# Kernel tuning notes

Measured on AMD Instinct MI355X. Metric: run time of the kernel, lower is better.

Reference implementation:

```python
import jax, jax.numpy as jnp
import numpy as np

HIDDEN = 160
LAYERS = 32
CLASSES = 10
IN_DIM = 784


def setup_inputs() -> dict:
    key = jax.random.key(0)
    ks = jax.random.split(key, 6)
    B = 65536
    x = jax.random.normal(ks[0], (B, IN_DIM), dtype=jnp.float32)
    # embed: torch nn.Linear(IN_DIM, HIDDEN); store weight as [IN_DIM, HIDDEN] so y = x @ W + b
    embed_w = jax.random.normal(ks[1], (IN_DIM, HIDDEN), dtype=jnp.float32) / np.sqrt(IN_DIM)
    embed_b = jnp.zeros((HIDDEN,), dtype=jnp.float32)
    # 32 residual-layer weights, kaiming_normal (fan_in=HIDDEN, relu gain sqrt(2)) scaled by 0.1
    layer_w = jax.random.normal(ks[2], (LAYERS, HIDDEN, HIDDEN), dtype=jnp.float32) * (np.sqrt(2.0 / HIDDEN) * 0.1)
    head_w = jax.random.normal(ks[3], (HIDDEN, CLASSES), dtype=jnp.float32) / np.sqrt(HIDDEN)
    head_b = jnp.zeros((CLASSES,), dtype=jnp.float32)
    return {"x": x, "embed_w": embed_w, "embed_b": embed_b,
            "layer_w": layer_w, "head_w": head_w, "head_b": head_b}


def reference(x, embed_w, embed_b, layer_w, head_w, head_b):
    # x: [B, 784] (already flat)
    h = x @ embed_w + embed_b  # [B, H]

    def step(h, W):
        # y = relu(h @ W) + h
        return jax.nn.relu(h @ W) + h, None

    h, _ = jax.lax.scan(step, h, layer_w)  # scan over the 32 layer weights
    return h @ head_w + head_b  # [B, CLASSES]
```

## Files before the change

### kernel.cpp

```cpp
#include <hip/hip_runtime.h>
#include <cstdint>
#include <cstddef>


typedef __attribute__((ext_vector_type(8))) short bfrag8;
typedef __attribute__((ext_vector_type(16))) float f32x16;
typedef __attribute__((ext_vector_type(4))) uint32_t u32x4;

#define MFMA32(a, b, c) __builtin_amdgcn_mfma_f32_32x32x16_bf16((a), (b), (c), 0, 0, 0)

#define NFRAG_TOTAL 1855
#define HALF_BYTES  25600
#define HALF_ELEMS  12800

#define WAITVM(N) asm volatile("s_waitcnt vmcnt(" #N ")" ::: "memory")

static __device__ __forceinline__ uint16_t f2bf16u(float v) {
    uint32_t u = __builtin_bit_cast(uint32_t, v);
    uint32_t r = u + 0x7FFFu + ((u >> 16) & 1u);
    return (uint16_t)(r >> 16);
}
static __device__ __forceinline__ uint32_t pack2_bf16(float lo, float hi) {
    return (uint32_t)f2bf16u(lo) | ((uint32_t)f2bf16u(hi) << 16);
}
static __device__ __forceinline__ uint32_t cvtpk(float lo, float hi) {
    uint32_t r;
    asm("v_cvt_pk_bf16_f32 %0, %1, %2" : "=v"(r) : "v"(lo), "v"(hi));
    return r;
}
static __device__ __forceinline__ void gl_lds16(const void* g, void* l) {
    __builtin_amdgcn_global_load_lds(
        (const __attribute__((address_space(1))) uint32_t*)g,
        (__attribute__((address_space(3))) uint32_t*)l, 16, 0, 0);
}

__global__ __launch_bounds__(256) void resmlp_prep(
    const float* __restrict__ embed_w, const float* __restrict__ layer_w,
    const float* __restrict__ head_w, uint16_t* __restrict__ ws)
{
    const int fb = blockIdx.x * 4 + (threadIdx.x >> 6);
    if (fb >= NFRAG_TOTAL) return;
    const int l = threadIdx.x & 63;
    const int h = l >> 5, m32 = l & 31;
    float v[8];
    if (fb < 245) {
        const int kt = fb / 5, mt = fb % 5;
        const int m = mt * 32 + m32;
        const int kb = kt * 16 + h * 8;
#pragma unroll
        for (int j = 0; j < 8; ++j)
            v[j] = embed_w[(size_t)(kb + j) * 160 + m];
    } else if (fb < 1845) {
        const int t = fb - 245, L = t / 50, r = t % 50, kt = r / 5, mt = r % 5;
        const int m = mt * 32 + m32;
        const float* W = layer_w + (size_t)L * 25600;
        const int kb = 32 * (kt >> 1) + 16 * (kt & 1) + 4 * h;
#pragma unroll
        for (int j = 0; j < 8; ++j)
            v[j] = W[(size_t)(kb + (j & 3) + 8 * (j >> 2)) * 160 + m];
    } else {
        const int kt = fb - 1845;
        const int kb = 32 * (kt >> 1) + 16 * (kt & 1) + 4 * h;
#pragma unroll
        for (int j = 0; j < 8; ++j)
            v[j] = (m32 < 10) ? head_w[(kb + (j & 3) + 8 * (j >> 2)) * 10 + m32] : 0.f;
    }
    u32x4 wv;
    wv.x = pack2_bf16(v[0], v[1]);
    wv.y = pack2_bf16(v[2], v[3]);
    wv.z = pack2_bf16(v[4], v[5]);
    wv.w = pack2_bf16(v[6], v[7]);
    *(u32x4*)((char*)ws + (size_t)fb * 1024 + l * 16) = wv;
}

template<int NK>
static __device__ __forceinline__ void embed_loadx(const float* __restrict__ xb,
                                                   float4 (&xv)[10])
{
#pragma unroll
    for (int kt = 0; kt < NK; ++kt) {
        xv[2 * kt]     = *(const float4*)(xb + kt * 16);
        xv[2 * kt + 1] = *(const float4*)(xb + kt * 16 + 4);
    }
}

template<int NK>
static __device__ __forceinline__ void embed_mfma_h(
    const uint16_t* __restrict__ buf, const float4 (&xv)[10],
    f32x16 (&acc)[5], int lane8)
{
    __builtin_amdgcn_s_setprio(1);
#pragma unroll
    for (int kt = 0; kt < NK; ++kt) {
        const float4 v0 = xv[2 * kt], v1 = xv[2 * kt + 1];
        u32x4 bw;
        bw.x = cvtpk(v0.x, v0.y);
        bw.y = cvtpk(v0.z, v0.w);
        bw.z = cvtpk(v1.x, v1.y);
        bw.w = cvtpk(v1.z, v1.w);
        const bfrag8 b = __builtin_bit_cast(bfrag8, bw);
#pragma unroll
        for (int mt = 0; mt < 5; ++mt) {
            const bfrag8 a = *(const bfrag8*)(buf + (kt * 5 + mt) * 512 + lane8);
            acc[mt] = MFMA32(a, b, acc[mt]);
        }
    }
    __builtin_amdgcn_s_setprio(0);
}

template<int KT0, int NMT, bool ZC>
static __device__ __forceinline__ void layer_mfma_h(
    const uint16_t* __restrict__ buf, f32x16 (&acc)[5],
    const f32x16 (&resid)[5], int lane8)
{
    __builtin_amdgcn_s_setprio(1);
#pragma unroll
    for (int i = 0; i < 5; ++i) {
        const int kt = KT0 + i, ms = kt >> 1, rb = (kt & 1) * 8;
        u32x4 bw;
        bw.x = cvtpk(resid[ms][rb + 0], resid[ms][rb + 1]);
        bw.y = cvtpk(resid[ms][rb + 2], resid[ms][rb + 3]);
        bw.z = cvtpk(resid[ms][rb + 4], resid[ms][rb + 5]);
        bw.w = cvtpk(resid[ms][rb + 6], resid[ms][rb + 7]);
        const bfrag8 b = __builtin_bit_cast(bfrag8, bw);
#pragma unroll
        for (int mt = 0; mt < NMT; ++mt) {
            const bfrag8 a = *(const bfrag8*)(buf + (i * NMT + mt) * 512 + lane8);
            if (ZC && i == 0) {
                f32x16 z;
#pragma unroll
                for (int r = 0; r < 16; ++r) z[r] = 0.f;
                acc[mt] = MFMA32(a, b, z);
            } else {
                acc[mt] = MFMA32(a, b, acc[mt]);
            }
        }
    }
    __builtin_amdgcn_s_setprio(0);
}

__global__ __launch_bounds__(256, 2) void resmlp_main(
    const float* __restrict__ x,
    const float* __restrict__ embed_b,
    const float* __restrict__ head_b,
    const uint16_t* __restrict__ ws,
    float* __restrict__ out)
{
    extern __shared__ __align__(16) uint16_t lds[];
    const int tid  = threadIdx.x;
    const int wave = tid >> 6, lane = tid & 63;
    const int hi = lane >> 5;
    const int lane8 = lane * 8;
    const int batch = blockIdx.x * 128 + wave * 32 + (lane & 31);

    f32x16 acc[5], resid[5];
#pragma unroll
    for (int mt = 0; mt < 5; ++mt)
#pragma unroll
        for (int r = 0; r < 16; ++r) acc[mt][r] = 0.f;

    auto do_stage = [&](int u) {
        int S, C;
        if (u < 10)      { S = (u >> 1) * 50 + (u & 1) * 25; C = (u == 9) ? 20 : 25; }
        else if (u < 74) { S = 245 + (u - 10) * 25;          C = 25; }
        else             { S = 1845 + (u - 74) * 5;          C = 5; }
        const char* src = (const char*)ws + (size_t)S * 1024 + lane * 16;
        char* dst = (char*)lds + (u % 3) * HALF_BYTES + lane * 16;
        for (int i = wave; i < C; i += 4)
            gl_lds16(src + (size_t)i * 1024, dst + i * 1024);
    };

    do_stage(0);
    do_stage(1);

    const float* xrow = x + (size_t)batch * 784 + hi * 8;

    for (int c = 0; c < 5; ++c) {
        float4 xv[10];
        __builtin_amdgcn_s_barrier();
        embed_loadx<5>(xrow + c * 160, xv);
        do_stage(2 * c + 2);
        WAITVM(11);
        embed_mfma_h<5>(lds + ((2 * c) % 3) * HALF_ELEMS, xv, acc, lane8);
        __builtin_amdgcn_s_barrier();
        if (c < 4) embed_loadx<5>(xrow + c * 160 + 80, xv);
        else       embed_loadx<4>(xrow + c * 160 + 80, xv);
        do_stage(2 * c + 3);
        WAITVM(11);
        if (c < 4) embed_mfma_h<5>(lds + ((2 * c + 1) % 3) * HALF_ELEMS, xv, acc, lane8);
        else       embed_mfma_h<4>(lds + ((2 * c + 1) % 3) * HALF_ELEMS, xv, acc, lane8);
    }

    for (int L = 0; L < 31; ++L) {
        const int u = 10 + 2 * L;
        const int bA = u % 3, bB = (u + 1) % 3;
        __builtin_amdgcn_s_barrier();
        do_stage(u + 2);
        if (L == 0) {
#pragma unroll
            for (int mt = 0; mt < 5; ++mt)
#pragma unroll
                for (int q2 = 0; q2 < 4; ++q2) {
                    const float4 b4 = *(const float4*)(embed_b + mt * 32 + q2 * 8 + hi * 4);
                    resid[mt][q2 * 4 + 0] = acc[mt][q2 * 4 + 0] + b4.x;
                    resid[mt][q2 * 4 + 1] = acc[mt][q2 * 4 + 1] + b4.y;
                    resid[mt][q2 * 4 + 2] = acc[mt][q2 * 4 + 2] + b4.z;
                    resid[mt][q2 * 4 + 3] = acc[mt][q2 * 4 + 3] + b4.w;
                }
        } else {
#pragma unroll
            for (int mt = 0; mt < 5; ++mt)
#pragma unroll
                for (int r = 0; r < 16; ++r)
                    resid[mt][r] += fmaxf(acc[mt][r], 0.f);
        }
        WAITVM(12);
        layer_mfma_h<0, 5, true>(lds + bA * HALF_ELEMS, acc, resid, lane8);
        __builtin_amdgcn_s_barrier();
        do_stage(u + 3);
        WAITVM(12);
        layer_mfma_h<5, 5, false>(lds + bB * HALF_ELEMS, acc, resid, lane8);
    }

    {
        __builtin_amdgcn_s_barrier();
        do_stage(74);
#pragma unroll
        for (int mt = 0; mt < 5; ++mt)
#pragma unroll
            for (int r = 0; r < 16; ++r)
                resid[mt][r] += fmaxf(acc[mt][r], 0.f);
        WAITVM(7);
        layer_mfma_h<0, 5, true>(lds + 0 * HALF_ELEMS, acc, resid, lane8);
        __builtin_amdgcn_s_barrier();
        do_stage(75);
        WAITVM(2);
        layer_mfma_h<5, 5, false>(lds + 1 * HALF_ELEMS, acc, resid, lane8);
    }

    {
        __builtin_amdgcn_s_barrier();
#pragma unroll
        for (int mt = 0; mt < 5; ++mt)
#pragma unroll
            for (int r = 0; r < 16; ++r)
                resid[mt][r] += fmaxf(acc[mt][r], 0.f);
        WAITVM(1);
        layer_mfma_h<0, 1, true>(lds + 2 * HALF_ELEMS, acc, resid, lane8);
        __builtin_amdgcn_s_barrier();
        WAITVM(0);
        layer_mfma_h<5, 1, false>(lds + 0 * HALF_ELEMS, acc, resid, lane8);
    }

    float* op = out + (size_t)batch * 10;
    if (hi == 0) {
        op[0] = acc[0][0] + head_b[0];
        op[1] = acc[0][1] + head_b[1];
        op[2] = acc[0][2] + head_b[2];
        op[3] = acc[0][3] + head_b[3];
        op[8] = acc[0][4] + head_b[8];
        op[9] = acc[0][5] + head_b[9];
    } else {
        op[4] = acc[0][0] + head_b[4];
        op[5] = acc[0][1] + head_b[5];
        op[6] = acc[0][2] + head_b[6];
        op[7] = acc[0][3] + head_b[7];
    }
}

extern "C" void kernel_launch(void* const* d_in, const int* in_sizes, int n_in,
                              void* d_out, int out_size, void* d_ws, size_t ws_size,
                              hipStream_t stream) {
    (void)in_sizes; (void)n_in; (void)out_size; (void)ws_size;
    const float* x       = (const float*)d_in[0];
    const float* embed_w = (const float*)d_in[1];
    const float* embed_b = (const float*)d_in[2];
    const float* layer_w = (const float*)d_in[3];
    const float* head_w  = (const float*)d_in[4];
    const float* head_b  = (const float*)d_in[5];
    float* out = (float*)d_out;

    uint16_t* ws = (uint16_t*)d_ws;

    const int dynLds = 3 * HALF_BYTES;
    (void)hipFuncSetAttribute((const void*)resmlp_main,
                              hipFuncAttributeMaxDynamicSharedMemorySize, dynLds);

    resmlp_prep<<<(NFRAG_TOTAL + 3) / 4, 256, 0, stream>>>(embed_w, layer_w, head_w, ws);
    resmlp_main<<<512, 256, dynLds, stream>>>(x, embed_b, head_b, ws, out);
}
```

Before: 398.8 us.

## Process two 32-row batch tiles per wave to reuse weight fragments across MFMAs

Each wave now handles 64 batch rows as two 32-row sub-tiles, so every LDS weight fragment read feeds two MFMAs instead of one. The block covers 256 rows, the grid is halved to 256 blocks, and occupancy drops to one block per CU. The LDS ring grows from three to six slots so a whole layer is staged ahead with one barrier per layer instead of two. In exchange, accumulator and residual register use roughly doubles, and the lower occupancy and single-block-per-CU schedule may expose more latency. The s_setprio hints are also removed.

```diff
diff --git a/kernel.cpp b/kernel.cpp
--- a/kernel.cpp
+++ b/kernel.cpp
@@ -10,8 +10,8 @@
 #define MFMA32(a, b, c) __builtin_amdgcn_mfma_f32_32x32x16_bf16((a), (b), (c), 0, 0, 0)
 
 #define NFRAG_TOTAL 1855
-#define HALF_BYTES  25600
-#define HALF_ELEMS  12800
+#define SLOT_BYTES  25600
+#define SLOT_ELEMS  12800
 
 #define WAITVM(N) asm volatile("s_waitcnt vmcnt(" #N ")" ::: "memory")
 
@@ -73,73 +73,68 @@
     *(u32x4*)((char*)ws + (size_t)fb * 1024 + l * 16) = wv;
 }
 
-template<int NK>
-static __device__ __forceinline__ void embed_loadx(const float* __restrict__ xb,
-                                                   float4 (&xv)[10])
-{
-#pragma unroll
-    for (int kt = 0; kt < NK; ++kt) {
-        xv[2 * kt]     = *(const float4*)(xb + kt * 16);
-        xv[2 * kt + 1] = *(const float4*)(xb + kt * 16 + 4);
-    }
-}
-
-template<int NK>
-static __device__ __forceinline__ void embed_mfma_h(
-    const uint16_t* __restrict__ buf, const float4 (&xv)[10],
-    f32x16 (&acc)[5], int lane8)
-{
-    __builtin_amdgcn_s_setprio(1);
-#pragma unroll
-    for (int kt = 0; kt < NK; ++kt) {
-        const float4 v0 = xv[2 * kt], v1 = xv[2 * kt + 1];
-        u32x4 bw;
-        bw.x = cvtpk(v0.x, v0.y);
-        bw.y = cvtpk(v0.z, v0.w);
-        bw.z = cvtpk(v1.x, v1.y);
-        bw.w = cvtpk(v1.z, v1.w);
-        const bfrag8 b = __builtin_bit_cast(bfrag8, bw);
+template<int NKT>
+static __device__ __forceinline__ void embed_half(
+    const uint16_t* __restrict__ buf,
+    const float* __restrict__ xr0, const float* __restrict__ xr1,
+    int kb, f32x16 (&acc)[2][5], int lane8)
+{
+#pragma unroll
+    for (int kt = 0; kt < NKT; ++kt) {
+        const float4 a0 = *(const float4*)(xr0 + kb + kt * 16);
+        const float4 a1 = *(const float4*)(xr0 + kb + kt * 16 + 4);
+        const float4 c0 = *(const float4*)(xr1 + kb + kt * 16);
+        const float4 c1 = *(const float4*)(xr1 + kb + kt * 16 + 4);
+        u32x4 w0, w1;
+        w0.x = cvtpk(a0.x, a0.y); w0.y = cvtpk(a0.z, a0.w);
+        w0.z = cvtpk(a1.x, a1.y); w0.w = cvtpk(a1.z, a1.w);
+        w1.x = cvtpk(c0.x, c0.y); w1.y = cvtpk(c0.z, c0.w);
+        w1.z = cvtpk(c1.x, c1.y); w1.w = cvtpk(c1.z, c1.w);
+        const bfrag8 b0 = __builtin_bit_cast(bfrag8, w0);
+        const bfrag8 b1 = __builtin_bit_cast(bfrag8, w1);
 #pragma unroll
         for (int mt = 0; mt < 5; ++mt) {
             const bfrag8 a = *(const bfrag8*)(buf + (kt * 5 + mt) * 512 + lane8);
-            acc[mt] = MFMA32(a, b, acc[mt]);
-        }
-    }
-    __builtin_amdgcn_s_setprio(0);
-}
-
-template<int KT0, int NMT, bool ZC>
-static __device__ __forceinline__ void layer_mfma_h(
-    const uint16_t* __restrict__ buf, f32x16 (&acc)[5],
-    const f32x16 (&resid)[5], int lane8)
-{
-    __builtin_amdgcn_s_setprio(1);
+            acc[0][mt] = MFMA32(a, b0, acc[0][mt]);
+            acc[1][mt] = MFMA32(a, b1, acc[1][mt]);
+        }
+    }
+}
+
+template<int KTB, int NMT, bool ZC>
+static __device__ __forceinline__ void layer_half(
+    const uint16_t* __restrict__ buf, f32x16 (&acc)[2][5],
+    const f32x16 (&resid)[2][5], const f32x16& zf, int lane8)
+{
 #pragma unroll
     for (int i = 0; i < 5; ++i) {
-        const int kt = KT0 + i, ms = kt >> 1, rb = (kt & 1) * 8;
-        u32x4 bw;
-        bw.x = cvtpk(resid[ms][rb + 0], resid[ms][rb + 1]);
-        bw.y = cvtpk(resid[ms][rb + 2], resid[ms][rb + 3]);
-        bw.z = cvtpk(resid[ms][rb + 4], resid[ms][rb + 5]);
-        bw.w = cvtpk(resid[ms][rb + 6], resid[ms][rb + 7]);
-        const bfrag8 b = __builtin_bit_cast(bfrag8, bw);
+        const int kt = KTB + i, ms = kt >> 1, rb = (kt & 1) * 8;
+        u32x4 w0, w1;
+        w0.x = cvtpk(resid[0][ms][rb + 0], resid[0][ms][rb + 1]);
+        w0.y = cvtpk(resid[0][ms][rb + 2], resid[0][ms][rb + 3]);
+        w0.z = cvtpk(resid[0][ms][rb + 4], resid[0][ms][rb + 5]);
+        w0.w = cvtpk(resid[0][ms][rb + 6], resid[0][ms][rb + 7]);
+        w1.x = cvtpk(resid[1][ms][rb + 0], resid[1][ms][rb + 1]);
+        w1.y = cvtpk(resid[1][ms][rb + 2], resid[1][ms][rb + 3]);
+        w1.z = cvtpk(resid[1][ms][rb + 4], resid[1][ms][rb + 5]);
+        w1.w = cvtpk(resid[1][ms][rb + 6], resid[1][ms][rb + 7]);
+        const bfrag8 b0 = __builtin_bit_cast(bfrag8, w0);
+        const bfrag8 b1 = __builtin_bit_cast(bfrag8, w1);
 #pragma unroll
         for (int mt = 0; mt < NMT; ++mt) {
             const bfrag8 a = *(const bfrag8*)(buf + (i * NMT + mt) * 512 + lane8);
             if (ZC && i == 0) {
-                f32x16 z;
-#pragma unroll
-                for (int r = 0; r < 16; ++r) z[r] = 0.f;
-                acc[mt] = MFMA32(a, b, z);
+                acc[0][mt] = MFMA32(a, b0, zf);
+                acc[1][mt] = MFMA32(a, b1, zf);
             } else {
-                acc[mt] = MFMA32(a, b, acc[mt]);
+                acc[0][mt] = MFMA32(a, b0, acc[0][mt]);
+                acc[1][mt] = MFMA32(a, b1, acc[1][mt]);
             }
         }
     }
-    __builtin_amdgcn_s_setprio(0);
-}
-
-__global__ __launch_bounds__(256, 2) void resmlp_main(
+}
+
+__global__ __launch_bounds__(256, 1) void resmlp_main(
     const float* __restrict__ x,
     const float* __restrict__ embed_b,
     const float* __restrict__ head_b,
@@ -149,122 +144,122 @@
     extern __shared__ __align__(16) uint16_t lds[];
     const int tid  = threadIdx.x;
     const int wave = tid >> 6, lane = tid & 63;
-    const int hi = lane >> 5;
+    const int hi = lane >> 5, ln = lane & 31;
     const int lane8 = lane * 8;
-    const int batch = blockIdx.x * 128 + wave * 32 + (lane & 31);
-
-    f32x16 acc[5], resid[5];
-#pragma unroll
-    for (int mt = 0; mt < 5; ++mt)
-#pragma unroll
-        for (int r = 0; r < 16; ++r) acc[mt][r] = 0.f;
-
-    auto do_stage = [&](int u) {
+    const int batch0 = blockIdx.x * 256 + wave * 64;
+    const float* xr0 = x + (size_t)(batch0 + ln) * 784 + hi * 8;
+    const float* xr1 = xr0 + (size_t)32 * 784;
+
+    f32x16 acc[2][5], resid[2][5];
+#pragma unroll
+    for (int s = 0; s < 2; ++s)
+#pragma unroll
+        for (int mt = 0; mt < 5; ++mt)
+#pragma unroll
+            for (int r = 0; r < 16; ++r) acc[s][mt][r] = 0.f;
+    f32x16 zf;
+#pragma unroll
+    for (int r = 0; r < 16; ++r) zf[r] = 0.f;
+
+    auto do_stage = [&](int u, int slot) {
         int S, C;
         if (u < 10)      { S = (u >> 1) * 50 + (u & 1) * 25; C = (u == 9) ? 20 : 25; }
         else if (u < 74) { S = 245 + (u - 10) * 25;          C = 25; }
-        else             { S = 1845 + (u - 74) * 5;          C = 5; }
+        else             { S = 1845 + (u - 74) * 5;          C = 5;  }
         const char* src = (const char*)ws + (size_t)S * 1024 + lane * 16;
-        char* dst = (char*)lds + (u % 3) * HALF_BYTES + lane * 16;
+        char* dst = (char*)lds + (size_t)slot * SLOT_BYTES + lane * 16;
         for (int i = wave; i < C; i += 4)
             gl_lds16(src + (size_t)i * 1024, dst + i * 1024);
     };
 
-    do_stage(0);
-    do_stage(1);
-
-    const float* xrow = x + (size_t)batch * 784 + hi * 8;
-
-    for (int c = 0; c < 5; ++c) {
-        float4 xv[10];
+    do_stage(0, 0);
+    WAITVM(0);
+    __builtin_amdgcn_s_barrier();
+
+    for (int e = 0; e < 8; ++e) {
+        do_stage(e + 1, (e + 1) % 6);
+        embed_half<5>(lds + (e % 6) * SLOT_ELEMS, xr0, xr1, e * 80, acc, lane8);
+        WAITVM(0);
         __builtin_amdgcn_s_barrier();
-        embed_loadx<5>(xrow + c * 160, xv);
-        do_stage(2 * c + 2);
-        WAITVM(11);
-        embed_mfma_h<5>(lds + ((2 * c) % 3) * HALF_ELEMS, xv, acc, lane8);
+    }
+    do_stage(9, 3);
+    embed_half<5>(lds + 2 * SLOT_ELEMS, xr0, xr1, 640, acc, lane8);
+    do_stage(10, 4);
+    do_stage(11, 5);
+    WAITVM(12);
+    __builtin_amdgcn_s_barrier();
+    embed_half<4>(lds + 3 * SLOT_ELEMS, xr0, xr1, 720, acc, lane8);
+    do_stage(12, 0);
+    do_stage(13, 1);
+    WAITVM(12);
+    __builtin_amdgcn_s_barrier();
+
+    int sA = 4, sS = 2, hS = 14;
+    for (int L = 0; L < 32; ++L) {
+        if (L <= 30) {
+            do_stage(hS, sS);
+            do_stage(hS + 1, sS + 1);
+        }
+        if (L == 0) {
+#pragma unroll
+            for (int s = 0; s < 2; ++s)
+#pragma unroll
+                for (int mt = 0; mt < 5; ++mt)
+#pragma unroll
+                    for (int q2 = 0; q2 < 4; ++q2) {
+                        const float4 b4 = *(const float4*)(embed_b + mt * 32 + q2 * 8 + hi * 4);
+                        resid[s][mt][q2 * 4 + 0] = acc[s][mt][q2 * 4 + 0] + b4.x;
+                        resid[s][mt][q2 * 4 + 1] = acc[s][mt][q2 * 4 + 1] + b4.y;
+                        resid[s][mt][q2 * 4 + 2] = acc[s][mt][q2 * 4 + 2] + b4.z;
+                        resid[s][mt][q2 * 4 + 3] = acc[s][mt][q2 * 4 + 3] + b4.w;
+                    }
+        } else {
+#pragma unroll
+            for (int s = 0; s < 2; ++s)
+#pragma unroll
+                for (int mt = 0; mt < 5; ++mt)
+#pragma unroll
+                    for (int r = 0; r < 16; ++r)
+                        resid[s][mt][r] += fmaxf(acc[s][mt][r], 0.f);
+        }
+        layer_half<0, 5, true >(lds + sA * SLOT_ELEMS, acc, resid, zf, lane8);
+        layer_half<5, 5, false>(lds + (sA + 1) * SLOT_ELEMS, acc, resid, zf, lane8);
+        if (L <= 29)      { WAITVM(12); }
+        else if (L == 30) { WAITVM(2);  }
+        else              { WAITVM(0);  }
         __builtin_amdgcn_s_barrier();
-        if (c < 4) embed_loadx<5>(xrow + c * 160 + 80, xv);
-        else       embed_loadx<4>(xrow + c * 160 + 80, xv);
-        do_stage(2 * c + 3);
-        WAITVM(11);
-        if (c < 4) embed_mfma_h<5>(lds + ((2 * c + 1) % 3) * HALF_ELEMS, xv, acc, lane8);
-        else       embed_mfma_h<4>(lds + ((2 * c + 1) % 3) * HALF_ELEMS, xv, acc, lane8);
-    }
-
-    for (int L = 0; L < 31; ++L) {
-        const int u = 10 + 2 * L;
-        const int bA = u % 3, bB = (u + 1) % 3;
-        __builtin_amdgcn_s_barrier();
-        do_stage(u + 2);
-        if (L == 0) {
-#pragma unroll
-            for (int mt = 0; mt < 5; ++mt)
-#pragma unroll
-                for (int q2 = 0; q2 < 4; ++q2) {
-                    const float4 b4 = *(const float4*)(embed_b + mt * 32 + q2 * 8 + hi * 4);
-                    resid[mt][q2 * 4 + 0] = acc[mt][q2 * 4 + 0] + b4.x;
-                    resid[mt][q2 * 4 + 1] = acc[mt][q2 * 4 + 1] + b4.y;
-                    resid[mt][q2 * 4 + 2] = acc[mt][q2 * 4 + 2] + b4.z;
-                    resid[mt][q2 * 4 + 3] = acc[mt][q2 * 4 + 3] + b4.w;
-                }
+        sA += 2; if (sA >= 6) sA -= 6;
+        sS += 2; if (sS >= 6) sS -= 6;
+        hS += 2;
+    }
+
+#pragma unroll
+    for (int s = 0; s < 2; ++s)
+#pragma unroll
+        for (int mt = 0; mt < 5; ++mt)
+#pragma unroll
+            for (int r = 0; r < 16; ++r)
+                resid[s][mt][r] += fmaxf(acc[s][mt][r], 0.f);
+    layer_half<0, 1, true >(lds + 2 * SLOT_ELEMS, acc, resid, zf, lane8);
+    layer_half<5, 1, false>(lds + 3 * SLOT_ELEMS, acc, resid, zf, lane8);
+
+#pragma unroll
+    for (int s = 0; s < 2; ++s) {
+        float* op = out + (size_t)(batch0 + s * 32 + ln) * 10;
+        const f32x16 a = acc[s][0];
+        if (hi == 0) {
+            op[0] = a[0] + head_b[0];
+            op[1] = a[1] + head_b[1];
+            op[2] = a[2] + head_b[2];
+            op[3] = a[3] + head_b[3];
+            op[8] = a[4] + head_b[8];
+            op[9] = a[5] + head_b[9];
         } else {
-#pragma unroll
-            for (int mt = 0; mt < 5; ++mt)
-#pragma unroll
-                for (int r = 0; r < 16; ++r)
-                    resid[mt][r] += fmaxf(acc[mt][r], 0.f);
-        }
-        WAITVM(12);
-        layer_mfma_h<0, 5, true>(lds + bA * HALF_ELEMS, acc, resid, lane8);
-        __builtin_amdgcn_s_barrier();
-        do_stage(u + 3);
-        WAITVM(12);
-        layer_mfma_h<5, 5, false>(lds + bB * HALF_ELEMS, acc, resid, lane8);
-    }
-
-    {
-        __builtin_amdgcn_s_barrier();
-        do_stage(74);
-#pragma unroll
-        for (int mt = 0; mt < 5; ++mt)
-#pragma unroll
-            for (int r = 0; r < 16; ++r)
-                resid[mt][r] += fmaxf(acc[mt][r], 0.f);
-        WAITVM(7);
-        layer_mfma_h<0, 5, true>(lds + 0 * HALF_ELEMS, acc, resid, lane8);
-        __builtin_amdgcn_s_barrier();
-        do_stage(75);
-        WAITVM(2);
-        layer_mfma_h<5, 5, false>(lds + 1 * HALF_ELEMS, acc, resid, lane8);
-    }
-
-    {
-        __builtin_amdgcn_s_barrier();
-#pragma unroll
-        for (int mt = 0; mt < 5; ++mt)
-#pragma unroll
-            for (int r = 0; r < 16; ++r)
-                resid[mt][r] += fmaxf(acc[mt][r], 0.f);
-        WAITVM(1);
-        layer_mfma_h<0, 1, true>(lds + 2 * HALF_ELEMS, acc, resid, lane8);
-        __builtin_amdgcn_s_barrier();
-        WAITVM(0);
-        layer_mfma_h<5, 1, false>(lds + 0 * HALF_ELEMS, acc, resid, lane8);
-    }
-
-    float* op = out + (size_t)batch * 10;
-    if (hi == 0) {
-        op[0] = acc[0][0] + head_b[0];
-        op[1] = acc[0][1] + head_b[1];
-        op[2] = acc[0][2] + head_b[2];
-        op[3] = acc[0][3] + head_b[3];
-        op[8] = acc[0][4] + head_b[8];
-        op[9] = acc[0][5] + head_b[9];
-    } else {
-        op[4] = acc[0][0] + head_b[4];
-        op[5] = acc[0][1] + head_b[5];
-        op[6] = acc[0][2] + head_b[6];
-        op[7] = acc[0][3] + head_b[7];
+            op[4] = a[0] + head_b[4];
+            op[5] = a[1] + head_b[5];
+            op[6] = a[2] + head_b[6];
+            op[7] = a[3] + head_b[7];
+        }
     }
 }
 
@@ -282,10 +277,10 @@
 
     uint16_t* ws = (uint16_t*)d_ws;
 
-    const int dynLds = 3 * HALF_BYTES;
+    const int dynLds = 6 * SLOT_BYTES;
     (void)hipFuncSetAttribute((const void*)resmlp_main,
                               hipFuncAttributeMaxDynamicSharedMemorySize, dynLds);
 
     resmlp_prep<<<(NFRAG_TOTAL + 3) / 4, 256, 0, stream>>>(embed_w, layer_w, head_w, ws);
-    resmlp_main<<<512, 256, dynLds, stream>>>(x, embed_b, head_b, ws, out);
-}
+    resmlp_main<<<256, 256, dynLds, stream>>>(x, embed_b, head_b, ws, out);
+}
```

After: 614.5 us. 1.54x slower.
